# Kernel tuning notes

Hardware: AMD Instinct MI355X
Metric: run time of the kernel (lower is better)

Reference implementation:

```python
import jax, jax.numpy as jnp
import numpy as np

B, S = 2, 1024
ENC_IN, MARK_IN = 21, 4
PRED_LEN, C_OUT = 96, 21
E = 512                 # embedding_dim
INNER = 2 * E           # proj_factor=2.0 (library default; Model does not pass it)
NH = 8                  # mLSTM heads
DH = INNER // NH        # 128
K = 4                   # causal conv1d kernel
BS = 4                  # qkv_proj_blocksize
NHP = INNER // BS       # 256 block-diagonal proj heads
NB = 4                  # num_blocks
EPS = 1e-5


def setup_inputs() -> dict:
    key = jax.random.key(0)
    ks = jax.random.split(key, 24)
    it = iter(range(24))
    def n(shape, s=0.02):
        return jax.random.normal(ks[next(it)], shape, jnp.float32) * s
    return {
        "x_enc": n((B, S, ENC_IN), 1.0),
        "x_mark_enc": n((B, S, MARK_IN), 1.0),
        "x_dec": n((B, PRED_LEN, ENC_IN), 1.0),
        "x_mark_dec": n((B, PRED_LEN, MARK_IN), 1.0),
        "emb_W": n((ENC_IN + MARK_IN, E), 0.05),
        "emb_b": jnp.zeros((E,), jnp.float32),
        "ln_w": jnp.ones((NB, E), jnp.float32),
        "up_W": n((NB, E, 2 * INNER)),
        "conv_W": n((NB, INNER, K), 0.1),
        "conv_b": jnp.zeros((NB, INNER), jnp.float32),
        "q_W": n((NB, NHP, BS, BS), 0.1),
        "k_W": n((NB, NHP, BS, BS), 0.1),
        "v_W": n((NB, NHP, BS, BS), 0.1),
        "ig_W": n((NB, 3 * INNER, NH)),
        "ig_b": jnp.zeros((NB, NH), jnp.float32),
        "fg_W": n((NB, 3 * INNER, NH)),
        "fg_b": jnp.tile(jnp.linspace(3.0, 6.0, NH, dtype=jnp.float32), (NB, 1)),
        "skip": jnp.ones((NB, INNER), jnp.float32),
        "onorm_w": jnp.ones((NB, INNER), jnp.float32),
        "down_W": n((NB, INNER, E)),
        "post_ln_w": jnp.ones((E,), jnp.float32),
        "head_W": n((E, C_OUT), 0.05),
        "head_b": jnp.zeros((C_OUT,), jnp.float32),
    }


def _ln(x, w):
    mu = jnp.mean(x, -1, keepdims=True)
    var = jnp.var(x, -1, keepdims=True)
    return (x - mu) * jax.lax.rsqrt(var + EPS) * w


def _headwise(x, w):
    # block-diagonal LinearHeadwiseExpand: (B,S,INNER) with (NHP,BS,BS) blocks
    xh = x.reshape(x.shape[0], x.shape[1], NHP, BS)
    return jnp.einsum('bshd,hod->bsho', xh, w).reshape(x.shape)


def _block(x, lw, uW, cW, cb, qW, kW, vW, igW, igb, fgW, fgb, sk, ow, dW):
    xn = _ln(x, lw)
    up = xn @ uW                                  # (B,S,2*INNER)
    xm, z = up[..., :INNER], up[..., INNER:]
    # causal depthwise conv1d + SiLU
    xc = jax.lax.conv_general_dilated(
        xm.transpose(0, 2, 1), cW[:, None, :], (1,), [(K - 1, 0)],
        feature_group_count=INNER,
        dimension_numbers=('NCH', 'OIH', 'NCH')).transpose(0, 2, 1) + cb
    xc = jax.nn.silu(xc)
    q = _headwise(xc, qW)
    k = _headwise(xc, kW)
    v = _headwise(xm, vW)
    qkv = jnp.concatenate([q, k, v], -1)          # (B,S,3*INNER)
    ig = (qkv @ igW + igb).transpose(0, 2, 1)     # (B,NH,S)
    fg = (qkv @ fgW + fgb).transpose(0, 2, 1)
    qh = q.reshape(B, S, NH, DH).transpose(0, 2, 1, 3)
    kh = k.reshape(B, S, NH, DH).transpose(0, 2, 1, 3)
    vh = v.reshape(B, S, NH, DH).transpose(0, 2, 1, 3)
    # parallel stabilized mLSTM (exp-gated linear attention)
    log_f = jax.nn.log_sigmoid(fg)
    cs = jnp.cumsum(log_f, -1)                    # (B,NH,S)
    Mmat = cs[..., :, None] - cs[..., None, :]    # (B,NH,S,S) cumulative decay
    tri = jnp.tril(jnp.ones((S, S), bool))
    logD = jnp.where(tri, Mmat + ig[..., None, :], -jnp.inf)
    m = jnp.max(logD, -1, keepdims=True)          # row-wise stabilizer
    D = jnp.exp(logD - m)
    qk = jnp.einsum('bnsd,bntd->bnst', qh, kh) / (DH ** 0.5)
    C = qk * D
    norm = jnp.maximum(jnp.abs(jnp.sum(C, -1, keepdims=True)), jnp.exp(-m))
    h = jnp.einsum('bnst,bntd->bnsd', C / (norm + 1e-6), vh)
    # multi-head layernorm (groupnorm over DH per head), weight, no bias
    hn = (h - jnp.mean(h, -1, keepdims=True)) * jax.lax.rsqrt(jnp.var(h, -1, keepdims=True) + EPS)
    hn = hn.transpose(0, 2, 1, 3).reshape(B, S, INNER) * ow
    hs = (hn + sk * xc) * jax.nn.silu(z)          # learnable skip + output gate
    return x + hs @ dW                            # residual


def reference(x_enc, x_mark_enc, x_dec, x_mark_dec, emb_W, emb_b, ln_w, up_W,
              conv_W, conv_b, q_W, k_W, v_W, ig_W, ig_b, fg_W, fg_b, skip,
              onorm_w, down_W, post_ln_w, head_W, head_b):
    x = jnp.concatenate([x_enc, x_mark_enc], -1) @ emb_W + emb_b
    for i in range(NB):
        x = _block(x, ln_w[i], up_W[i], conv_W[i], conv_b[i], q_W[i], k_W[i],
                   v_W[i], ig_W[i], ig_b[i], fg_W[i], fg_b[i], skip[i],
                   onorm_w[i], down_W[i])
    x = _ln(x, post_ln_w)
    return x[:, -PRED_LEN:, :] @ head_W + head_b
```

## Files before the change

kernel.cpp:

```cpp
#include <hip/hip_runtime.h>
#include <hip/hip_bf16.h>

#define S_LEN 1024
#define E_DIM 512
#define INNER_D 1024
#define NHEAD 8
#define DHEAD 128

typedef unsigned short u16;
typedef unsigned int u32;
typedef __attribute__((ext_vector_type(8))) short short8;
typedef __attribute__((ext_vector_type(4))) float f32x4;

union S8 { short8 v; u16 u[8]; uint4 q; };

__device__ __forceinline__ u16 f2bf(float f) {
  u32 u = __float_as_uint(f);
  u32 r = u + 0x7FFFu + ((u >> 16) & 1u);
  return (u16)(r >> 16);
}
__device__ __forceinline__ float bf2f(u16 u) { return __uint_as_float(((u32)u) << 16); }

__device__ __forceinline__ void gload16(const u16* g, u16* l) {
  __builtin_amdgcn_global_load_lds((const __attribute__((address_space(1))) void*)g,
                                   (__attribute__((address_space(3))) void*)l, 16, 0, 0);
}

__device__ __forceinline__ void prep_transpose(
    const float* __restrict__ in, u16* __restrict__ out, int K, int N,
    int k0, int n0, int t, u16 (*T)[72])
{
  int kr = t >> 2, nseg = (t & 3) * 16;
  const float* src = in + (size_t)(k0 + kr) * N + n0 + nseg;
#pragma unroll
  for (int j = 0; j < 16; j++) T[kr][nseg + j] = f2bf(src[j]);
  __syncthreads();
  int nr = t >> 2, kseg = (t & 3) * 16;
  u32 u[8];
#pragma unroll
  for (int rr = 0; rr < 8; rr++) {
    u32 lo = T[kseg + 2 * rr][nr];
    u32 hi = T[kseg + 2 * rr + 1][nr];
    u[rr] = lo | (hi << 16);
  }
  u16* dst = out + (size_t)(n0 + nr) * K + k0 + kseg;
  uint4 w0 = {u[0], u[1], u[2], u[3]};
  uint4 w1 = {u[4], u[5], u[6], u[7]};
  *(uint4*)dst = w0;
  *(uint4*)(dst + 8) = w1;
}

__global__ __launch_bounds__(256) void prep_kernel(
    const float* __restrict__ up_W, u16* __restrict__ upWt,
    const float* __restrict__ down_W, u16* __restrict__ dnWt,
    const float* __restrict__ igW, const float* __restrict__ fgW,
    u16* __restrict__ ghi, u16* __restrict__ glo,
    const float* __restrict__ xe, const float* __restrict__ xmk,
    const float* __restrict__ eW, const float* __restrict__ eb,
    float* __restrict__ x)
{
  __shared__ u16 T[64][72];
  __shared__ float in_s[25];
  int id = blockIdx.x;
  int t = threadIdx.x;
  if (id < 1024) {
    int bx = id & 7, rest = id >> 3;
    int by = rest & 31, L = rest >> 5;
    prep_transpose(up_W + (size_t)L * 512 * 2048, upWt + (size_t)L * 1048576,
                   512, 2048, bx * 64, by * 64, t, T);
  } else if (id < 1536) {
    int id2 = id - 1024;
    int bx = id2 & 15, rest = id2 >> 4;
    int by = rest & 7, L = rest >> 3;
    prep_transpose(down_W + (size_t)L * 1024 * 512, dnWt + (size_t)L * 524288,
                   1024, 512, bx * 64, by * 64, t, T);
  } else if (id < 2304) {
    int id3 = id - 1536;
    int bx = id3 % 12, rest = id3 / 12;
    int n = rest & 15, L = rest >> 4;
    int k = bx * 256 + t;
    const float* W = ((n < 8) ? igW : fgW) + (size_t)L * 24576;
    float v = W[(size_t)k * 8 + (n & 7)];
    u16 h = f2bf(v);
    u16 l = f2bf(v - bf2f(h));
    size_t o = ((size_t)L * 16 + n) * 3072 + k;
    ghi[o] = h;
    glo[o] = l;
  } else {
    int row = id - 2304;
    if (t < 21) in_s[t] = xe[row * 21 + t];
    else if (t < 25) in_s[t] = xmk[row * 4 + t - 21];
    __syncthreads();
#pragma unroll
    for (int rep = 0; rep < 2; rep++) {
      int e = t + rep * 256;
      float acc = eb[e];
#pragma unroll
      for (int i = 0; i < 25; i++) acc += in_s[i] * eW[i * E_DIM + e];
      x[(size_t)row * E_DIM + e] = acc;
    }
  }
}

__global__ __launch_bounds__(256) void ln_kernel(
    const float* __restrict__ x, const float* __restrict__ w, u16* __restrict__ out)
{
  int row = blockIdx.x, tid = threadIdx.x;
  const float* xr = x + (size_t)row * E_DIM;
  float2 v = *(const float2*)(xr + tid * 2);
  float s = v.x + v.y, q = v.x * v.x + v.y * v.y;
#pragma unroll
  for (int off = 32; off; off >>= 1) { s += __shfl_xor(s, off); q += __shfl_xor(q, off); }
  __shared__ float ssum[4], ssq[4];
  int wv = tid >> 6;
  if ((tid & 63) == 0) { ssum[wv] = s; ssq[wv] = q; }
  __syncthreads();
  s = ssum[0] + ssum[1] + ssum[2] + ssum[3];
  q = ssq[0] + ssq[1] + ssq[2] + ssq[3];
  float mu = s * (1.f / E_DIM);
  float var = q * (1.f / E_DIM) - mu * mu;
  float rs = rsqrtf(var + 1e-5f);
  int e = tid * 2;
  ushort2 o;
  o.x = f2bf((v.x - mu) * rs * w[e]);
  o.y = f2bf((v.y - mu) * rs * w[e + 1]);
  *(ushort2*)(out + (size_t)row * E_DIM + e) = o;
}

__global__ __launch_bounds__(256) void lnhead_kernel(
    const float* __restrict__ x, const float* __restrict__ w,
    const float* __restrict__ hW, const float* __restrict__ hb,
    float* __restrict__ out)
{
  int ridx = blockIdx.x;
  int b = ridx / 96, r = ridx % 96;
  int row = b * S_LEN + (S_LEN - 96) + r;
  int tid = threadIdx.x;
  const float* xr = x + (size_t)row * E_DIM;
  float2 v = *(const float2*)(xr + tid * 2);
  float s = v.x + v.y, q = v.x * v.x + v.y * v.y;
#pragma unroll
  for (int off = 32; off; off >>= 1) { s += __shfl_xor(s, off); q += __shfl_xor(q, off); }
  __shared__ float ssum[4], ssq[4];
  __shared__ float lnv[512];
  __shared__ float part[8][32];
  int wv = tid >> 6;
  if ((tid & 63) == 0) { ssum[wv] = s; ssq[wv] = q; }
  __syncthreads();
  s = ssum[0] + ssum[1] + ssum[2] + ssum[3];
  q = ssq[0] + ssq[1] + ssq[2] + ssq[3];
  float mu = s * (1.f / E_DIM);
  float var = q * (1.f / E_DIM) - mu * mu;
  float rs = rsqrtf(var + 1e-5f);
  int e = tid * 2;
  lnv[e]     = (v.x - mu) * rs * w[e];
  lnv[e + 1] = (v.y - mu) * rs * w[e + 1];
  __syncthreads();
  int n = tid & 31, sl = tid >> 5;
  float p = 0.f;
  if (n < 21) {
#pragma unroll 8
    for (int kk = 0; kk < 64; kk++)
      p += lnv[sl * 64 + kk] * hW[(sl * 64 + kk) * 21 + n];
  }
  part[sl][n] = p;
  __syncthreads();
  if (tid < 21) {
    float acc = hb[tid];
#pragma unroll
    for (int j = 0; j < 8; j++) acc += part[j][tid];
    out[ridx * 21 + tid] = acc;
  }
}

__global__ __launch_bounds__(256) void gemm_bf16_split64(
    const u16* __restrict__ A, const u16* __restrict__ Bt,
    float* __restrict__ C0, u16* __restrict__ C1,
    int M, int N, int K, int split_col, int ldc)
{
  __shared__ u16 As0[128 * 64], As1[128 * 64], As2[128 * 64];
  __shared__ u16 Bs0[128 * 64], Bs1[128 * 64], Bs2[128 * 64];
  const int tid = threadIdx.x;
  const int row0 = blockIdx.y * 128, col0 = blockIdx.x * 128;
  const int wave = tid >> 6, lane = tid & 63;
  const int wr = wave >> 1, wc = wave & 1;
  const int lm = lane & 15, lq = lane >> 4;
  const int lr8 = lane >> 3;
  const int cg8 = (lane & 7) ^ lr8;
  f32x4 acc[4][4] = {};
  const u16* Abase = A + (size_t)(row0 + lr8) * K + cg8 * 8;
  const u16* Bbase = Bt + (size_t)(col0 + lr8) * K + cg8 * 8;
  const int key = lm & 7;

#define STG_UP(AS, BS, K0) do { \
  _Pragma("unroll") for (int i = 0; i < 4; i++) \
    gload16(Abase + (size_t)((wave * 4 + i) * 8) * K + (K0), &AS[(wave * 4 + i) * 512]); \
  _Pragma("unroll") for (int i = 0; i < 4; i++) \
    gload16(Bbase + (size_t)((wave * 4 + i) * 8) * K + (K0), &BS[(wave * 4 + i) * 512]); \
} while (0)

#define CMP_UP(AS, BS) do { \
  _Pragma("unroll") for (int kc = 0; kc < 2; kc++) { \
    short8 af[4], bfv[4]; \
    _Pragma("unroll") for (int i = 0; i < 4; i++) \
      af[i] = *(const short8*)&AS[(wr * 64 + i * 16 + lm) * 64 + (((kc * 4 + lq) ^ key) * 8)]; \
    _Pragma("unroll") for (int j = 0; j < 4; j++) \
      bfv[j] = *(const short8*)&BS[(wc * 64 + j * 16 + lm) * 64 + (((kc * 4 + lq) ^ key) * 8)]; \
    _Pragma("unroll") for (int i = 0; i < 4; i++) \
      _Pragma("unroll") for (int j = 0; j < 4; j++) \
        acc[i][j] = __builtin_amdgcn_mfma_f32_16x16x32_bf16(af[i], bfv[j], acc[i][j], 0, 0, 0); \
  } \
} while (0)

  STG_UP(As0, Bs0, 0);
  asm volatile("" ::: "memory");
  STG_UP(As1, Bs1, 64);
  asm volatile("" ::: "memory");
  STG_UP(As2, Bs2, 128);
#pragma unroll
  for (int t = 0; t < 8; t++) {
    if (t <= 5)       asm volatile("s_waitcnt vmcnt(16)" ::: "memory");
    else if (t == 6)  asm volatile("s_waitcnt vmcnt(8)" ::: "memory");
    else              asm volatile("s_waitcnt vmcnt(0)" ::: "memory");
    __builtin_amdgcn_sched_barrier(0);
    __builtin_amdgcn_s_barrier();
    if ((t % 3) == 0)      CMP_UP(As0, Bs0);
    else if ((t % 3) == 1) CMP_UP(As1, Bs1);
    else                   CMP_UP(As2, Bs2);
    __builtin_amdgcn_s_barrier();
    if (t + 3 < 8) {
      if ((t % 3) == 0)      STG_UP(As0, Bs0, (t + 3) * 64);
      else if ((t % 3) == 1) STG_UP(As1, Bs1, (t + 3) * 64);
      else                   STG_UP(As2, Bs2, (t + 3) * 64);
    }
  }
#undef STG_UP
#undef CMP_UP

  const bool toC1 = (col0 >= split_col);
#pragma unroll
  for (int i = 0; i < 4; i++) {
#pragma unroll
    for (int j = 0; j < 4; j++) {
      int col = col0 - (toC1 ? split_col : 0) + wc * 64 + j * 16 + lm;
#pragma unroll
      for (int r = 0; r < 4; r++) {
        int row = row0 + wr * 64 + i * 16 + lq * 4 + r;
        if (toC1) C1[(size_t)row * ldc + col] = f2bf(acc[i][j][r]);
        else C0[(size_t)row * ldc + col] = acc[i][j][r];
      }
    }
  }
}

__global__ __launch_bounds__(256) void gemm_bf16_32(
    const u16* __restrict__ A, const u16* __restrict__ Bt,
    float* __restrict__ C, int M, int N, int K, int ldc)
{
  __shared__ u16 As0[64 * 128], As1[64 * 128], As2[64 * 128];
  __shared__ u16 Bs0[64 * 128], Bs1[64 * 128], Bs2[64 * 128];
  const int tid = threadIdx.x;
  const int row0 = blockIdx.y * 64, col0 = blockIdx.x * 64;
  const int wave = tid >> 6, lane = tid & 63;
  const int wr = wave >> 1, wc = wave & 1;
  const int lm = lane & 15, lq = lane >> 4;
  const int lr16 = lane >> 4;
  const int ls16 = lane & 15;
  f32x4 acc[2][2] = {};

#define STAGE_DN(AS, BS, K0) do { \
  _Pragma("unroll") for (int i = 0; i < 4; i++) { \
    int rA = (wave * 4 + i) * 4 + lr16; \
    int cgk = ls16 ^ (rA & 15); \
    gload16(A + (size_t)(row0 + rA) * K + (K0) + cgk * 8, &AS[(wave * 4 + i) * 512]); \
  } \
  _Pragma("unroll") for (int i = 0; i < 4; i++) { \
    int rB = (wave * 4 + i) * 4 + lr16; \
    int cgk = ls16 ^ (rB & 15); \
    gload16(Bt + (size_t)(col0 + rB) * K + (K0) + cgk * 8, &BS[(wave * 4 + i) * 512]); \
  } \
} while (0)

#define COMPUTE_DN(AS, BS) do { \
  _Pragma("unroll") for (int kc = 0; kc < 4; kc++) { \
    short8 af[2], bfv[2]; \
    _Pragma("unroll") for (int i = 0; i < 2; i++) \
      af[i] = *(const short8*)&AS[(wr * 32 + i * 16 + lm) * 128 + (((kc * 4 + lq) ^ lm) * 8)]; \
    _Pragma("unroll") for (int j = 0; j < 2; j++) \
      bfv[j] = *(const short8*)&BS[(wc * 32 + j * 16 + lm) * 128 + (((kc * 4 + lq) ^ lm) * 8)]; \
    _Pragma("unroll") for (int i = 0; i < 2; i++) \
      _Pragma("unroll") for (int j = 0; j < 2; j++) \
        acc[i][j] = __builtin_amdgcn_mfma_f32_16x16x32_bf16(af[i], bfv[j], acc[i][j], 0, 0, 0); \
  } \
} while (0)

  STAGE_DN(As0, Bs0, 0);
  asm volatile("" ::: "memory");
  STAGE_DN(As1, Bs1, 128);
  asm volatile("" ::: "memory");
  STAGE_DN(As2, Bs2, 256);
#pragma unroll
  for (int t = 0; t < 8; t++) {
    if (t <= 5)       asm volatile("s_waitcnt vmcnt(16)" ::: "memory");
    else if (t == 6)  asm volatile("s_waitcnt vmcnt(8)" ::: "memory");
    else              asm volatile("s_waitcnt vmcnt(0)" ::: "memory");
    __builtin_amdgcn_sched_barrier(0);
    __builtin_amdgcn_s_barrier();
    if ((t % 3) == 0)      COMPUTE_DN(As0, Bs0);
    else if ((t % 3) == 1) COMPUTE_DN(As1, Bs1);
    else                   COMPUTE_DN(As2, Bs2);
    __builtin_amdgcn_s_barrier();
    if (t + 3 < 8) {
      if ((t % 3) == 0)      STAGE_DN(As0, Bs0, (t + 3) * 128);
      else if ((t % 3) == 1) STAGE_DN(As1, Bs1, (t + 3) * 128);
      else                   STAGE_DN(As2, Bs2, (t + 3) * 128);
    }
  }
#undef STAGE_DN
#undef COMPUTE_DN

#pragma unroll
  for (int i = 0; i < 2; i++) {
#pragma unroll
    for (int j = 0; j < 2; j++) {
      int col = col0 + wc * 32 + j * 16 + lm;
#pragma unroll
      for (int r = 0; r < 4; r++) {
        int row = row0 + wr * 32 + i * 16 + lq * 4 + r;
        C[(size_t)row * ldc + col] += acc[i][j][r];
      }
    }
  }
}

__global__ __launch_bounds__(256) void convqkv_kernel(
    const float* __restrict__ xm,
    const float* __restrict__ cw, const float* __restrict__ cb,
    const float* __restrict__ qw, const float* __restrict__ kw, const float* __restrict__ vw,
    float* __restrict__ xc, u16* __restrict__ q, u16* __restrict__ k, u16* __restrict__ v,
    u16* __restrict__ vt)
{
  int r0 = blockIdx.x * 8;
  int s0 = r0 & (S_LEN - 1);
  int g = threadIdx.x;
  int c0 = g * 4;
  const float* base = xm + (size_t)r0 * INNER_D + c0;

  float4 xv[11];
#pragma unroll
  for (int j = 0; j < 11; j++) {
    int ts = s0 - 3 + j;
    float4 t = {0.f, 0.f, 0.f, 0.f};
    if (ts >= 0) t = *(const float4*)(base + (ptrdiff_t)(j - 3) * INNER_D);
    xv[j] = t;
  }
  float cwv[4][4];
#pragma unroll
  for (int c = 0; c < 4; c++)
#pragma unroll
    for (int kk = 0; kk < 4; kk++) cwv[c][kk] = cw[(c0 + c) * 4 + kk];
  float cbv[4] = {cb[c0], cb[c0 + 1], cb[c0 + 2], cb[c0 + 3]};
  const float* qg = qw + g * 16;
  const float* kg = kw + g * 16;
  const float* vg = vw + g * 16;
  float qwv[16], kwv[16], vwv[16];
#pragma unroll
  for (int i = 0; i < 16; i++) { qwv[i] = qg[i]; kwv[i] = kg[i]; vwv[i] = vg[i]; }

  u32 vt_pack[4][4];

#pragma unroll
  for (int i = 0; i < 8; i++) {
    float a0 = cbv[0], a1 = cbv[1], a2 = cbv[2], a3 = cbv[3];
#pragma unroll
    for (int kk = 0; kk < 4; kk++) {
      float4 xvv = xv[i + kk];
      a0 += xvv.x * cwv[0][kk];
      a1 += xvv.y * cwv[1][kk];
      a2 += xvv.z * cwv[2][kk];
      a3 += xvv.w * cwv[3][kk];
    }
    a0 = a0 / (1.f + __expf(-a0));
    a1 = a1 / (1.f + __expf(-a1));
    a2 = a2 / (1.f + __expf(-a2));
    a3 = a3 / (1.f + __expf(-a3));
    float4 accv = {a0, a1, a2, a3};
    *(float4*)(xc + (size_t)(r0 + i) * INNER_D + c0) = accv;

    float xcv[4] = {a0, a1, a2, a3};
    float xmv[4] = {xv[i + 3].x, xv[i + 3].y, xv[i + 3].z, xv[i + 3].w};
    ushort4 qs, ks, vs;
    u16* qp = (u16*)&qs; u16* kp = (u16*)&ks; u16* vp = (u16*)&vs;
#pragma unroll
    for (int o = 0; o < 4; o++) {
      float aq = 0.f, ak = 0.f, av = 0.f;
#pragma unroll
      for (int d = 0; d < 4; d++) {
        aq += xcv[d] * qwv[o * 4 + d];
        ak += xcv[d] * kwv[o * 4 + d];
        av += xmv[d] * vwv[o * 4 + d];
      }
      qp[o] = f2bf(aq); kp[o] = f2bf(ak);
      u16 vv = f2bf(av);
      vp[o] = vv;
      if ((i & 1) == 0) vt_pack[o][i >> 1] = (u32)vv;
      else              vt_pack[o][i >> 1] |= ((u32)vv) << 16;
    }
    size_t off = (size_t)(r0 + i) * INNER_D + c0;
    *(ushort4*)(q + off) = qs;
    *(ushort4*)(k + off) = ks;
    *(ushort4*)(v + off) = vs;
  }
  u16* vtb = vt + ((size_t)((r0 >> 10) * INNER_D + c0)) * S_LEN + s0;
#pragma unroll
  for (int c = 0; c < 4; c++) {
    uint4 wv4 = {vt_pack[c][0], vt_pack[c][1], vt_pack[c][2], vt_pack[c][3]};
    *(uint4*)(vtb + (size_t)c * S_LEN) = wv4;
  }
}

__global__ __launch_bounds__(256) void gates_mfma_kernel(
    const u16* __restrict__ q, const u16* __restrict__ k, const u16* __restrict__ v,
    const u16* __restrict__ whi, const u16* __restrict__ wlo,
    const float* __restrict__ igb, const float* __restrict__ fgb,
    float* __restrict__ ig, float* __restrict__ fg)
{
  const int blk2 = blockIdx.x;
  const int blk = blk2 >> 1, half = blk2 & 1;
  const int tid = threadIdx.x;
  const int wave = tid >> 6, lane = tid & 63;
  const int lm = lane & 15, lq = lane >> 4;
  const int grow = blk * 16 + lm;
  const u16* parts[3] = {q, k, v};
  f32x4 acc = {};
#pragma unroll 4
  for (int kc = 0; kc < 12; kc++) {
    int k0 = half * 1536 + wave * 384 + kc * 32;
    int part = k0 >> 10;
    int idx = (k0 & 1023) + lq * 8;
    S8 a, bh_, bl_;
    a.q = *(const uint4*)(parts[part] + (size_t)grow * INNER_D + idx);
    bh_.q = *(const uint4*)(whi + (size_t)lm * 3072 + k0 + lq * 8);
    bl_.q = *(const uint4*)(wlo + (size_t)lm * 3072 + k0 + lq * 8);
    __builtin_amdgcn_s_setprio(1);
    acc = __builtin_amdgcn_mfma_f32_16x16x32_bf16(a.v, bh_.v, acc, 0, 0, 0);
    acc = __builtin_amdgcn_mfma_f32_16x16x32_bf16(a.v, bl_.v, acc, 0, 0, 0);
    __builtin_amdgcn_s_setprio(0);
  }
  __shared__ float red[4][16][17];
#pragma unroll
  for (int r = 0; r < 4; r++) red[wave][lq * 4 + r][lm] = acc[r];
  __syncthreads();
  if (wave == 0) {
#pragma unroll
    for (int r = 0; r < 4; r++) {
      int row = lq * 4 + r;
      float sum = red[0][row][lm] + red[1][row][lm] + red[2][row][lm] + red[3][row][lm];
      int growr = blk * 16 + row;
      int b = growr >> 10, s = growr & (S_LEN - 1);
      if (lm < 8) {
        float bias = (half == 0) ? igb[lm] : 0.f;
        ig[half * 16384 + ((size_t)(b * NHEAD + lm) << 10) + s] = sum + bias;
      } else {
        float bias = (half == 0) ? fgb[lm - 8] : 0.f;
        fg[half * 16384 + ((size_t)(b * NHEAD + (lm - 8)) << 10) + s] = sum + bias;
      }
    }
  }
}

__global__ __launch_bounds__(1024) void scan_kernel(
    const float* __restrict__ ig, const float* __restrict__ fg,
    float* __restrict__ a, float* __restrict__ rm, float* __restrict__ enm)
{
  int bh = blockIdx.x;
  int t = threadIdx.x;
  int lane = t & 63, wv = t >> 6;
  __shared__ float sw[16];
  size_t o = ((size_t)bh << 10) + t;
  float f = fg[o] + fg[16384 + o];
  float lf = (f >= 0.f) ? -log1pf(__expf(-f)) : f - log1pf(__expf(f));
  float v = lf;
#pragma unroll
  for (int off = 1; off < 64; off <<= 1) {
    float u = __shfl_up(v, off);
    if (lane >= off) v += u;
  }
  if (lane == 63) sw[wv] = v;
  __syncthreads();
  float pre = 0.f;
  for (int w = 0; w < wv; w++) pre += sw[w];
  float cs = v + pre;
  float av = (ig[o] + ig[16384 + o]) - cs;
  a[o] = __expf(av);
  float m = av;
#pragma unroll
  for (int off = 1; off < 64; off <<= 1) {
    float u = __shfl_up(m, off);
    if (lane >= off) m = fmaxf(m, u);
  }
  __syncthreads();
  if (lane == 63) sw[wv] = m;
  __syncthreads();
  float pm = -3.4e38f;
  for (int w = 0; w < wv; w++) pm = fmaxf(pm, sw[w]);
  float rmx = fmaxf(m, pm);
  rm[o] = rmx;
  enm[o] = __expf(-(cs + rmx));
}

__device__ __constant__ int c_qp[15] = {7, 7, 7, 6, 6, 6, 5, 5, 4, 4, 3, 3, 2, 1, 0};
__device__ __constant__ int c_k0[15] = {0, 6,11, 0, 5,10, 0, 6, 0, 5, 0, 4, 0, 0, 0};
__device__ __constant__ int c_k1[15] = {6,11,16, 5,10,14, 6,12, 5,10, 4, 8, 6, 4, 2};
__device__ __constant__ int c_md[15] = {1, 2, 3, 1, 2, 3, 1, 2, 1, 2, 1, 2, 0, 0, 0};

#define HP_SLOT 1310720
#define SC_SLOT 10240

__global__ __launch_bounds__(512) void attn_mfma_kernel(
    const u16* __restrict__ qhg, const u16* __restrict__ khg, const u16* __restrict__ vtg,
    const float* __restrict__ a_arr, const float* __restrict__ rm_arr, const float* __restrict__ enm_arr,
    const float* __restrict__ xc, const u16* __restrict__ zh,
    const float* __restrict__ skip, const float* __restrict__ onw,
    u16* __restrict__ hs, float* __restrict__ hpart, float* __restrict__ scpart)
{
  const int bh = blockIdx.x;
  const int job = blockIdx.y;
  const int qp = c_qp[job], k0t = c_k0[job], k1t = c_k1[job], mode = c_md[job];
  const int b = bh >> 3, h = bh & 7;
  const int s0 = qp * 128;
  const int tid = threadIdx.x;
  const int wave = tid >> 6, lane = tid & 63;
  const int lm = lane & 15, lq = lane >> 4;
  const size_t rowbase = (size_t)b * S_LEN;
  const int c0 = h * DHEAD;

  __shared__ u16 Ks0[64 * 128], Ks1[64 * 128];
  __shared__ u16 Vt0[128 * 64], Vt1[128 * 64];
  __shared__ u16 Ws[128 * 72];

  short8 aq[4];
  {
    const u16* qpp = qhg + (rowbase + s0 + wave * 16 + lm) * INNER_D + c0 + lq * 8;
#pragma unroll
    for (int kc = 0; kc < 4; kc++) {
      S8 tmp; tmp.q = *(const uint4*)(qpp + kc * 32);
      aq[kc] = tmp.v;
    }
  }
  const float scale = 0.08838834764831845f;
  float rmv[4], er[4];
#pragma unroll
  for (int r = 0; r < 4; r++) {
    rmv[r] = rm_arr[(size_t)bh * S_LEN + s0 + wave * 16 + lq * 4 + r];
    er[r] = scale * __expf(-rmv[r]);
  }

  S8 onesu;
#pragma unroll
  for (int j = 0; j < 8; j++) onesu.u[j] = 0x3F80;
  const short8 ones8 = onesu.v;

  f32x4 accH[8] = {};
  f32x4 accS = {};
  const int lr16 = lane >> 4;
  const int ls16 = lane & 15;
  const int lr8 = lane >> 3;
  const int cgv = (lane & 7) ^ lr8;
  const u16* vtbase = vtg + ((size_t)b * INNER_D + c0) * S_LEN;

  float ae0[4], ae1[4];

#define PREF(KS, VS, AE, T0) do { \
  _Pragma("unroll") for (int j = 0; j < 2; j++) { \
    int rK = (wave * 2 + j) * 4 + lr16; \
    int cgk = ls16 ^ (rK & 7); \
    gload16(khg + (rowbase + (T0) + rK) * INNER_D + c0 + cgk * 8, &KS[(wave * 2 + j) * 512]); \
  } \
  _Pragma("unroll") for (int j = 0; j < 2; j++) { \
    int rV = (wave * 2 + j) * 8 + lr8; \
    gload16(vtbase + (size_t)rV * S_LEN + (T0) + cgv * 8, &VS[(wave * 2 + j) * 512]); \
  } \
  _Pragma("unroll") for (int cb = 0; cb < 4; cb++) \
    AE[cb] = a_arr[(size_t)bh * S_LEN + (T0) + cb * 16 + lm]; \
} while (0)

#define QK_STEP(KS, PACC) do { \
  __builtin_amdgcn_s_setprio(1); \
  _Pragma("unroll") for (int kc = 0; kc < 4; kc++) \
    _Pragma("unroll") for (int cb = 0; cb < 4; cb++) { \
      short8 bk = *(const short8*)&KS[(cb * 16 + lm) * 128 + (((kc * 4 + lq) ^ (lm & 7)) * 8)]; \
      PACC[cb] = __builtin_amdgcn_mfma_f32_16x16x32_bf16(aq[kc], bk, PACC[cb], 0, 0, 0); \
    } \
  __builtin_amdgcn_s_setprio(0); \
} while (0)

#define W_PV(AE, VT, T0, PACC, MSK) do { \
  _Pragma("unroll") for (int cb = 0; cb < 4; cb++) { \
    float ec = AE[cb]; \
    _Pragma("unroll") for (int r = 0; r < 4; r++) { \
      float wv = PACC[cb][r] * ec * er[r]; \
      if (MSK) { \
        int colg = (T0) + cb * 16 + lm; \
        int rowg = s0 + wave * 16 + lq * 4 + r; \
        if (colg > rowg) wv = 0.f; \
      } \
      Ws[(wave * 16 + lq * 4 + r) * 72 + cb * 16 + lm] = f2bf(wv); \
    } \
  } \
  __builtin_amdgcn_s_setprio(1); \
  _Pragma("unroll") for (int kc = 0; kc < 2; kc++) { \
    short8 aw = *(const short8*)&Ws[(wave * 16 + lm) * 72 + kc * 32 + lq * 8]; \
    accS = __builtin_amdgcn_mfma_f32_16x16x32_bf16(aw, ones8, accS, 0, 0, 0); \
    _Pragma("unroll") for (int nb = 0; nb < 8; nb++) { \
      short8 bv = *(const short8*)&VT[(nb * 16 + lm) * 64 + (((kc * 4 + lq) ^ (lm & 7)) * 8)]; \
      accH[nb] = __builtin_amdgcn_mfma_f32_16x16x32_bf16(aw, bv, accH[nb], 0, 0, 0); \
    } \
  } \
  __builtin_amdgcn_s_setprio(0); \
} while (0)

  int kt = k0t;
  PREF(Ks0, Vt0, ae0, kt * 64);
  asm volatile("" ::: "memory");
  if (kt + 1 < k1t) PREF(Ks1, Vt1, ae1, (kt + 1) * 64);

  while (true) {
    {
      if (kt + 1 < k1t) asm volatile("s_waitcnt vmcnt(8)" ::: "memory");
      else              asm volatile("s_waitcnt vmcnt(0)" ::: "memory");
      __builtin_amdgcn_sched_barrier(0);
      __builtin_amdgcn_s_barrier();
      f32x4 pacc[4] = {};
      QK_STEP(Ks0, pacc);
      bool msk = (kt * 64 >= s0);
      W_PV(ae0, Vt0, kt * 64, pacc, msk);
      __builtin_amdgcn_s_barrier();
      if (kt + 2 < k1t) PREF(Ks0, Vt0, ae0, (kt + 2) * 64);
      kt++;
      if (kt >= k1t) break;
    }
    {
      if (kt + 1 < k1t) asm volatile("s_waitcnt vmcnt(8)" ::: "memory");
      else              asm volatile("s_waitcnt vmcnt(0)" ::: "memory");
      __builtin_amdgcn_sched_barrier(0);
      __builtin_amdgcn_s_barrier();
      f32x4 pacc[4] = {};
      QK_STEP(Ks1, pacc);
      bool msk = (kt * 64 >= s0);
      W_PV(ae1, Vt1, kt * 64, pacc, msk);
      __builtin_amdgcn_s_barrier();
      if (kt + 2 < k1t) PREF(Ks1, Vt1, ae1, (kt + 2) * 64);
      kt++;
      if (kt >= k1t) break;
    }
  }
#undef PREF
#undef QK_STEP
#undef W_PV

  if (mode != 0) {
    int slot = mode - 1;
    int qr = qp - 3;
    float* Hp = hpart + (size_t)slot * HP_SLOT + ((size_t)(bh * 5 + qr)) * 16384;
    float* sp = scpart + slot * SC_SLOT + (bh * 5 + qr) * 128;
#pragma unroll
    for (int r = 0; r < 4; r++) {
      int row = wave * 16 + lq * 4 + r;
      if (lm == 0) sp[row] = accS[r];
#pragma unroll
      for (int nb = 0; nb < 8; nb++)
        Hp[row * 128 + nb * 16 + lm] = accH[nb][r];
    }
    return;
  }

  float inv[4], muv[4], rsv[4];
#pragma unroll
  for (int r = 0; r < 4; r++) {
    int rowg = s0 + wave * 16 + lq * 4 + r;
    float nrm = fmaxf(fabsf(accS[r]), enm_arr[(size_t)bh * S_LEN + rowg]);
    inv[r] = 1.f / (nrm + 1e-6f);
  }
#pragma unroll
  for (int r = 0; r < 4; r++) {
    float s = 0.f, qq = 0.f;
#pragma unroll
    for (int nb = 0; nb < 8; nb++) {
      float hv = accH[nb][r] * inv[r];
      accH[nb][r] = hv;
      s += hv; qq += hv * hv;
    }
    s += __shfl_xor(s, 1); s += __shfl_xor(s, 2); s += __shfl_xor(s, 4); s += __shfl_xor(s, 8);
    qq += __shfl_xor(qq, 1); qq += __shfl_xor(qq, 2); qq += __shfl_xor(qq, 4); qq += __shfl_xor(qq, 8);
    float mu = s * (1.f / DHEAD);
    float var = qq * (1.f / DHEAD) - mu * mu;
    muv[r] = mu;
    rsv[r] = rsqrtf(var + 1e-5f);
  }
  float ow[8], sk[8];
#pragma unroll
  for (int nb = 0; nb < 8; nb++) {
    ow[nb] = onw[c0 + nb * 16 + lm];
    sk[nb] = skip[c0 + nb * 16 + lm];
  }
#pragma unroll
  for (int r = 0; r < 4; r++) {
    int rowg = s0 + wave * 16 + lq * 4 + r;
    size_t base = (rowbase + rowg) * INNER_D + c0;
#pragma unroll
    for (int nb = 0; nb < 8; nb++) {
      int d = nb * 16 + lm;
      float xcv = xc[base + d];
      float zv = bf2f(zh[base + d]);
      float hn = (accH[nb][r] - muv[r]) * rsv[r] * ow[nb] + sk[nb] * xcv;
      float o = hn * (zv / (1.f + __expf(-zv)));
      hs[base + d] = f2bf(o);
    }
  }
}

__global__ __launch_bounds__(256) void attn_combine_kernel(
    const float* __restrict__ hpart, const float* __restrict__ scpart,
    const float* __restrict__ enm,
    const float* __restrict__ xc, const u16* __restrict__ zh,
    const float* __restrict__ skip, const float* __restrict__ onw,
    u16* __restrict__ hs)
{
  int wave = threadIdx.x >> 6, lane = threadIdx.x & 63;
  int gid = blockIdx.x * 4 + wave;
  int bh = gid / 640;
  int rr = gid % 640;
  int qr = rr >> 7, row = rr & 127;
  int b = bh >> 3, hh = bh & 7;
  int s = (qr + 3) * 128 + row;
  int nsl = (qr >= 3) ? 3 : 2;
  size_t off = (((size_t)(bh * 5 + qr)) * 128 + row) * 128 + lane * 2;
  int sidx = (bh * 5 + qr) * 128 + row;
  float hx = 0.f, hy = 0.f, sc = 0.f;
  for (int sl = 0; sl < nsl; sl++) {
    float2 hp = *(const float2*)(hpart + (size_t)sl * HP_SLOT + off);
    hx += hp.x; hy += hp.y;
    sc += scpart[sl * SC_SLOT + sidx];
  }
  float nrm = fmaxf(fabsf(sc), enm[(size_t)bh * S_LEN + s]);
  float inv = 1.f / (nrm + 1e-6f);
  hx *= inv; hy *= inv;
  float sm = hx + hy, sq = hx * hx + hy * hy;
#pragma unroll
  for (int off2 = 32; off2; off2 >>= 1) { sm += __shfl_xor(sm, off2); sq += __shfl_xor(sq, off2); }
  float mu = sm * (1.f / DHEAD);
  float var = sq * (1.f / DHEAD) - mu * mu;
  float rs = rsqrtf(var + 1e-5f);
  int c0 = hh * DHEAD + lane * 2;
  size_t base = ((size_t)(b * S_LEN + s)) * INNER_D + c0;
  float2 xc2 = *(const float2*)(xc + base);
  ushort2 z2u = *(const ushort2*)(zh + base);
  float z2x = bf2f(z2u.x), z2y = bf2f(z2u.y);
  float skx = skip[c0], sky = skip[c0 + 1];
  float owx = onw[c0],  owy = onw[c0 + 1];
  ushort2 o;
  o.x = f2bf(((hx - mu) * rs * owx + skx * xc2.x) * (z2x / (1.f + __expf(-z2x))));
  o.y = f2bf(((hy - mu) * rs * owy + sky * xc2.y) * (z2y / (1.f + __expf(-z2y))));
  *(ushort2*)(hs + base) = o;
}

extern "C" void kernel_launch(void* const* d_in, const int* in_sizes, int n_in,
                              void* d_out, int out_size, void* d_ws, size_t ws_size,
                              hipStream_t stream)
{
  const float* x_enc   = (const float*)d_in[0];
  const float* x_mark  = (const float*)d_in[1];
  const float* emb_W   = (const float*)d_in[4];
  const float* emb_b   = (const float*)d_in[5];
  const float* ln_w    = (const float*)d_in[6];
  const float* up_W    = (const float*)d_in[7];
  const float* conv_W  = (const float*)d_in[8];
  const float* conv_b  = (const float*)d_in[9];
  const float* q_W     = (const float*)d_in[10];
  const float* k_W     = (const float*)d_in[11];
  const float* v_W     = (const float*)d_in[12];
  const float* ig_W    = (const float*)d_in[13];
  const float* ig_b    = (const float*)d_in[14];
  const float* fg_W    = (const float*)d_in[15];
  const float* fg_b    = (const float*)d_in[16];
  const float* skip_w  = (const float*)d_in[17];
  const float* onorm_w = (const float*)d_in[18];
  const float* down_W  = (const float*)d_in[19];
  const float* post_ln = (const float*)d_in[20];
  const float* head_W  = (const float*)d_in[21];
  const float* head_b  = (const float*)d_in[22];

  float* p = (float*)d_ws;
  float* x    = p; p += 1048576;
  float* xm   = p; p += 2097152;
  float* xc   = p; p += 2097152;
  float* igb_ = p; p += 32768;
  float* fgb_ = p; p += 32768;
  float* ab   = p; p += 16384;
  float* rmb  = p; p += 16384;
  float* enmb = p; p += 16384;
  u16* qhb = (u16*)p; p += 1048576;
  u16* khb = (u16*)p; p += 1048576;
  u16* vhb = (u16*)p; p += 1048576;
  u16* zh  = (u16*)p; p += 1048576;
  u16* xnh = (u16*)p; p += 524288;
  u16* upWtA = (u16*)p; p += 2097152;
  u16* dnWtA = (u16*)p; p += 1048576;
  u16* gtwH = (u16*)p; p += 98304;
  u16* gtwL = (u16*)p; p += 98304;
  float* hpart = p; p += 3932160;
  float* scpart = p; p += 32768;
  u16* vtg = (u16*)p; p += 1048576;
  u16* hsbh = (u16*)xm;

  prep_kernel<<<4352, 256, 0, stream>>>(
      up_W, upWtA, down_W, dnWtA, ig_W, fg_W, gtwH, gtwL,
      x_enc, x_mark, emb_W, emb_b, x);

  for (int L = 0; L < 4; L++) {
    ln_kernel<<<2048, 256, 0, stream>>>(x, ln_w + L * 512, xnh);
    gemm_bf16_split64<<<dim3(16, 16), 256, 0, stream>>>(
        xnh, upWtA + (size_t)L * 1048576, xm, zh, 2048, 2048, 512, 1024, 1024);
    convqkv_kernel<<<256, 256, 0, stream>>>(
        xm, conv_W + L * 4096, conv_b + L * 1024,
        q_W + L * 4096, k_W + L * 4096, v_W + L * 4096,
        xc, qhb, khb, vhb, vtg);
    gates_mfma_kernel<<<256, 256, 0, stream>>>(
        qhb, khb, vhb, gtwH + (size_t)L * 49152, gtwL + (size_t)L * 49152,
        ig_b + L * 8, fg_b + L * 8, igb_, fgb_);
    scan_kernel<<<16, 1024, 0, stream>>>(igb_, fgb_, ab, rmb, enmb);
    attn_mfma_kernel<<<dim3(16, 15), 512, 0, stream>>>(
        qhb, khb, vtg, ab, rmb, enmb, xc, zh,
        skip_w + L * 1024, onorm_w + L * 1024, hsbh, hpart, scpart);
    attn_combine_kernel<<<2560, 256, 0, stream>>>(
        hpart, scpart, enmb, xc, zh, skip_w + L * 1024, onorm_w + L * 1024, hsbh);
    gemm_bf16_32<<<dim3(8, 32), 256, 0, stream>>>(
        hsbh, dnWtA + (size_t)L * 524288, x, 2048, 512, 1024, 512);
  }

  lnhead_kernel<<<192, 256, 0, stream>>>(x, post_ln, head_W, head_b, (float*)d_out);
}
```

Measured before the change: 415.5 us.

## Fuse gate scan into attention kernel and vectorize layernorm rows per wave

Removes the separate scan_kernel launch: every attention block recomputes the forget-gate cumulative sum, decay exponentials and running max for its head in shared memory, and stores the stabilizer only for its own query tile. Decay factors are read from LDS instead of being prefetched from global memory, so the vmcnt wait counts are lowered. The layernorm kernel now handles one row per wave with float4 loads and 16-byte stores, using a quarter of the blocks. The trade-off is redundant scan work across the 15 job blocks per head and more LDS use, in exchange for one fewer launch and fewer global round trips per layer.

```diff
diff --git a/kernel.cpp b/kernel.cpp
--- a/kernel.cpp
+++ b/kernel.cpp
@@ -105,26 +105,30 @@
 __global__ __launch_bounds__(256) void ln_kernel(
     const float* __restrict__ x, const float* __restrict__ w, u16* __restrict__ out)
 {
-  int row = blockIdx.x, tid = threadIdx.x;
-  const float* xr = x + (size_t)row * E_DIM;
-  float2 v = *(const float2*)(xr + tid * 2);
-  float s = v.x + v.y, q = v.x * v.x + v.y * v.y;
-#pragma unroll
-  for (int off = 32; off; off >>= 1) { s += __shfl_xor(s, off); q += __shfl_xor(q, off); }
-  __shared__ float ssum[4], ssq[4];
-  int wv = tid >> 6;
-  if ((tid & 63) == 0) { ssum[wv] = s; ssq[wv] = q; }
-  __syncthreads();
-  s = ssum[0] + ssum[1] + ssum[2] + ssum[3];
-  q = ssq[0] + ssq[1] + ssq[2] + ssq[3];
+  int row = blockIdx.x * 4 + (threadIdx.x >> 6);
+  int lane = threadIdx.x & 63;
+  const float* xr = x + (size_t)row * E_DIM + lane * 8;
+  float4 a = *(const float4*)xr;
+  float4 b = *(const float4*)(xr + 4);
+  float s = a.x + a.y + a.z + a.w + b.x + b.y + b.z + b.w;
+  float q = a.x * a.x + a.y * a.y + a.z * a.z + a.w * a.w
+          + b.x * b.x + b.y * b.y + b.z * b.z + b.w * b.w;
+#pragma unroll
+  for (int off = 1; off < 64; off <<= 1) { s += __shfl_xor(s, off); q += __shfl_xor(q, off); }
   float mu = s * (1.f / E_DIM);
   float var = q * (1.f / E_DIM) - mu * mu;
   float rs = rsqrtf(var + 1e-5f);
-  int e = tid * 2;
-  ushort2 o;
-  o.x = f2bf((v.x - mu) * rs * w[e]);
-  o.y = f2bf((v.y - mu) * rs * w[e + 1]);
-  *(ushort2*)(out + (size_t)row * E_DIM + e) = o;
+  const float* wr = w + lane * 8;
+  S8 o;
+  o.u[0] = f2bf((a.x - mu) * rs * wr[0]);
+  o.u[1] = f2bf((a.y - mu) * rs * wr[1]);
+  o.u[2] = f2bf((a.z - mu) * rs * wr[2]);
+  o.u[3] = f2bf((a.w - mu) * rs * wr[3]);
+  o.u[4] = f2bf((b.x - mu) * rs * wr[4]);
+  o.u[5] = f2bf((b.y - mu) * rs * wr[5]);
+  o.u[6] = f2bf((b.z - mu) * rs * wr[6]);
+  o.u[7] = f2bf((b.w - mu) * rs * wr[7]);
+  *(uint4*)(out + (size_t)row * E_DIM + lane * 8) = o.q;
 }
 
 __global__ __launch_bounds__(256) void lnhead_kernel(
@@ -469,46 +473,6 @@
   }
 }
 
-__global__ __launch_bounds__(1024) void scan_kernel(
-    const float* __restrict__ ig, const float* __restrict__ fg,
-    float* __restrict__ a, float* __restrict__ rm, float* __restrict__ enm)
-{
-  int bh = blockIdx.x;
-  int t = threadIdx.x;
-  int lane = t & 63, wv = t >> 6;
-  __shared__ float sw[16];
-  size_t o = ((size_t)bh << 10) + t;
-  float f = fg[o] + fg[16384 + o];
-  float lf = (f >= 0.f) ? -log1pf(__expf(-f)) : f - log1pf(__expf(f));
-  float v = lf;
-#pragma unroll
-  for (int off = 1; off < 64; off <<= 1) {
-    float u = __shfl_up(v, off);
-    if (lane >= off) v += u;
-  }
-  if (lane == 63) sw[wv] = v;
-  __syncthreads();
-  float pre = 0.f;
-  for (int w = 0; w < wv; w++) pre += sw[w];
-  float cs = v + pre;
-  float av = (ig[o] + ig[16384 + o]) - cs;
-  a[o] = __expf(av);
-  float m = av;
-#pragma unroll
-  for (int off = 1; off < 64; off <<= 1) {
-    float u = __shfl_up(m, off);
-    if (lane >= off) m = fmaxf(m, u);
-  }
-  __syncthreads();
-  if (lane == 63) sw[wv] = m;
-  __syncthreads();
-  float pm = -3.4e38f;
-  for (int w = 0; w < wv; w++) pm = fmaxf(pm, sw[w]);
-  float rmx = fmaxf(m, pm);
-  rm[o] = rmx;
-  enm[o] = __expf(-(cs + rmx));
-}
-
 __device__ __constant__ int c_qp[15] = {7, 7, 7, 6, 6, 6, 5, 5, 4, 4, 3, 3, 2, 1, 0};
 __device__ __constant__ int c_k0[15] = {0, 6,11, 0, 5,10, 0, 6, 0, 5, 0, 4, 0, 0, 0};
 __device__ __constant__ int c_k1[15] = {6,11,16, 5,10,14, 6,12, 5,10, 4, 8, 6, 4, 2};
@@ -519,10 +483,11 @@
 
 __global__ __launch_bounds__(512) void attn_mfma_kernel(
     const u16* __restrict__ qhg, const u16* __restrict__ khg, const u16* __restrict__ vtg,
-    const float* __restrict__ a_arr, const float* __restrict__ rm_arr, const float* __restrict__ enm_arr,
+    const float* __restrict__ ig_arr, const float* __restrict__ fg_arr,
     const float* __restrict__ xc, const u16* __restrict__ zh,
     const float* __restrict__ skip, const float* __restrict__ onw,
-    u16* __restrict__ hs, float* __restrict__ hpart, float* __restrict__ scpart)
+    u16* __restrict__ hs, float* __restrict__ hpart, float* __restrict__ scpart,
+    float* __restrict__ enmp)
 {
   const int bh = blockIdx.x;
   const int job = blockIdx.y;
@@ -538,6 +503,9 @@
   __shared__ u16 Ks0[64 * 128], Ks1[64 * 128];
   __shared__ u16 Vt0[128 * 64], Vt1[128 * 64];
   __shared__ u16 Ws[128 * 72];
+  __shared__ float sa[1024];
+  __shared__ float sws[16], swm[16];
+  __shared__ float srm[128], senm[128];
 
   short8 aq[4];
   {
@@ -548,11 +516,65 @@
       aq[kc] = tmp.v;
     }
   }
+
+  {
+    float vsc[2], igv[2], css[2], msc[2];
+#pragma unroll
+    for (int c = 0; c < 2; c++) {
+      int vt = c * 512 + tid;
+      size_t o = ((size_t)bh << 10) + vt;
+      float f = fg_arr[o] + fg_arr[16384 + o];
+      igv[c] = ig_arr[o] + ig_arr[16384 + o];
+      float lf = (f >= 0.f) ? -log1pf(__expf(-f)) : f - log1pf(__expf(f));
+      float v = lf;
+#pragma unroll
+      for (int off = 1; off < 64; off <<= 1) {
+        float u = __shfl_up(v, off);
+        if (lane >= off) v += u;
+      }
+      if (lane == 63) sws[c * 8 + (tid >> 6)] = v;
+      vsc[c] = v;
+    }
+    __syncthreads();
+#pragma unroll
+    for (int c = 0; c < 2; c++) {
+      int vt = c * 512 + tid;
+      int wvv = c * 8 + (tid >> 6);
+      float pre = 0.f;
+      for (int u = 0; u < wvv; u++) pre += sws[u];
+      float cs = vsc[c] + pre;
+      float av = igv[c] - cs;
+      sa[vt] = __expf(av);
+      float m = av;
+#pragma unroll
+      for (int off = 1; off < 64; off <<= 1) {
+        float u = __shfl_up(m, off);
+        if (lane >= off) m = fmaxf(m, u);
+      }
+      if (lane == 63) swm[wvv] = m;
+      css[c] = cs; msc[c] = m;
+    }
+    __syncthreads();
+#pragma unroll
+    for (int c = 0; c < 2; c++) {
+      int vt = c * 512 + tid;
+      int wvv = c * 8 + (tid >> 6);
+      float pm = -3.4e38f;
+      for (int u = 0; u < wvv; u++) pm = fmaxf(pm, swm[u]);
+      float rmx = fmaxf(msc[c], pm);
+      if (vt >= s0 && vt < s0 + 128) {
+        srm[vt - s0] = rmx;
+        senm[vt - s0] = __expf(-(css[c] + rmx));
+      }
+    }
+    __syncthreads();
+  }
+
   const float scale = 0.08838834764831845f;
   float rmv[4], er[4];
 #pragma unroll
   for (int r = 0; r < 4; r++) {
-    rmv[r] = rm_arr[(size_t)bh * S_LEN + s0 + wave * 16 + lq * 4 + r];
+    rmv[r] = srm[wave * 16 + lq * 4 + r];
     er[r] = scale * __expf(-rmv[r]);
   }
 
@@ -569,9 +591,7 @@
   const int cgv = (lane & 7) ^ lr8;
   const u16* vtbase = vtg + ((size_t)b * INNER_D + c0) * S_LEN;
 
-  float ae0[4], ae1[4];
-
-#define PREF(KS, VS, AE, T0) do { \
+#define PREF(KS, VS, T0) do { \
   _Pragma("unroll") for (int j = 0; j < 2; j++) { \
     int rK = (wave * 2 + j) * 4 + lr16; \
     int cgk = ls16 ^ (rK & 7); \
@@ -581,8 +601,6 @@
     int rV = (wave * 2 + j) * 8 + lr8; \
     gload16(vtbase + (size_t)rV * S_LEN + (T0) + cgv * 8, &VS[(wave * 2 + j) * 512]); \
   } \
-  _Pragma("unroll") for (int cb = 0; cb < 4; cb++) \
-    AE[cb] = a_arr[(size_t)bh * S_LEN + (T0) + cb * 16 + lm]; \
 } while (0)
 
 #define QK_STEP(KS, PACC) do { \
@@ -595,9 +613,9 @@
   __builtin_amdgcn_s_setprio(0); \
 } while (0)
 
-#define W_PV(AE, VT, T0, PACC, MSK) do { \
+#define W_PV(VT, T0, PACC, MSK) do { \
   _Pragma("unroll") for (int cb = 0; cb < 4; cb++) { \
-    float ec = AE[cb]; \
+    float ec = sa[(T0) + cb * 16 + lm]; \
     _Pragma("unroll") for (int r = 0; r < 4; r++) { \
       float wv = PACC[cb][r] * ec * er[r]; \
       if (MSK) { \
@@ -621,36 +639,36 @@
 } while (0)
 
   int kt = k0t;
-  PREF(Ks0, Vt0, ae0, kt * 64);
+  PREF(Ks0, Vt0, kt * 64);
   asm volatile("" ::: "memory");
-  if (kt + 1 < k1t) PREF(Ks1, Vt1, ae1, (kt + 1) * 64);
+  if (kt + 1 < k1t) PREF(Ks1, Vt1, (kt + 1) * 64);
 
   while (true) {
     {
-      if (kt + 1 < k1t) asm volatile("s_waitcnt vmcnt(8)" ::: "memory");
+      if (kt + 1 < k1t) asm volatile("s_waitcnt vmcnt(4)" ::: "memory");
       else              asm volatile("s_waitcnt vmcnt(0)" ::: "memory");
       __builtin_amdgcn_sched_barrier(0);
       __builtin_amdgcn_s_barrier();
       f32x4 pacc[4] = {};
       QK_STEP(Ks0, pacc);
       bool msk = (kt * 64 >= s0);
-      W_PV(ae0, Vt0, kt * 64, pacc, msk);
+      W_PV(Vt0, kt * 64, pacc, msk);
       __builtin_amdgcn_s_barrier();
-      if (kt + 2 < k1t) PREF(Ks0, Vt0, ae0, (kt + 2) * 64);
+      if (kt + 2 < k1t) PREF(Ks0, Vt0, (kt + 2) * 64);
       kt++;
       if (kt >= k1t) break;
     }
     {
-      if (kt + 1 < k1t) asm volatile("s_waitcnt vmcnt(8)" ::: "memory");
+      if (kt + 1 < k1t) asm volatile("s_waitcnt vmcnt(4)" ::: "memory");
       else              asm volatile("s_waitcnt vmcnt(0)" ::: "memory");
       __builtin_amdgcn_sched_barrier(0);
       __builtin_amdgcn_s_barrier();
       f32x4 pacc[4] = {};
       QK_STEP(Ks1, pacc);
       bool msk = (kt * 64 >= s0);
-      W_PV(ae1, Vt1, kt * 64, pacc, msk);
+      W_PV(Vt1, kt * 64, pacc, msk);
       __builtin_amdgcn_s_barrier();
-      if (kt + 2 < k1t) PREF(Ks1, Vt1, ae1, (kt + 2) * 64);
+      if (kt + 2 < k1t) PREF(Ks1, Vt1, (kt + 2) * 64);
       kt++;
       if (kt >= k1t) break;
     }
@@ -664,10 +682,14 @@
     int qr = qp - 3;
     float* Hp = hpart + (size_t)slot * HP_SLOT + ((size_t)(bh * 5 + qr)) * 16384;
     float* sp = scpart + slot * SC_SLOT + (bh * 5 + qr) * 128;
+    float* ep = enmp + (bh * 5 + qr) * 128;
 #pragma unroll
     for (int r = 0; r < 4; r++) {
       int row = wave * 16 + lq * 4 + r;
-      if (lm == 0) sp[row] = accS[r];
+      if (lm == 0) {
+        sp[row] = accS[r];
+        if (slot == 0) ep[row] = senm[row];
+      }
 #pragma unroll
       for (int nb = 0; nb < 8; nb++)
         Hp[row * 128 + nb * 16 + lm] = accH[nb][r];
@@ -678,8 +700,8 @@
   float inv[4], muv[4], rsv[4];
 #pragma unroll
   for (int r = 0; r < 4; r++) {
-    int rowg = s0 + wave * 16 + lq * 4 + r;
-    float nrm = fmaxf(fabsf(accS[r]), enm_arr[(size_t)bh * S_LEN + rowg]);
+    int row = wave * 16 + lq * 4 + r;
+    float nrm = fmaxf(fabsf(accS[r]), senm[row]);
     inv[r] = 1.f / (nrm + 1e-6f);
   }
 #pragma unroll
@@ -722,7 +744,7 @@
 
 __global__ __launch_bounds__(256) void attn_combine_kernel(
     const float* __restrict__ hpart, const float* __restrict__ scpart,
-    const float* __restrict__ enm,
+    const float* __restrict__ enmp,
     const float* __restrict__ xc, const u16* __restrict__ zh,
     const float* __restrict__ skip, const float* __restrict__ onw,
     u16* __restrict__ hs)
@@ -743,7 +765,7 @@
     hx += hp.x; hy += hp.y;
     sc += scpart[sl * SC_SLOT + sidx];
   }
-  float nrm = fmaxf(fabsf(sc), enm[(size_t)bh * S_LEN + s]);
+  float nrm = fmaxf(fabsf(sc), enmp[sidx]);
   float inv = 1.f / (nrm + 1e-6f);
   hx *= inv; hy *= inv;
   float sm = hx + hy, sq = hx * hx + hy * hy;
@@ -797,9 +819,7 @@
   float* xc   = p; p += 2097152;
   float* igb_ = p; p += 32768;
   float* fgb_ = p; p += 32768;
-  float* ab   = p; p += 16384;
-  float* rmb  = p; p += 16384;
-  float* enmb = p; p += 16384;
+  float* enmp = p; p += 16384;
   u16* qhb = (u16*)p; p += 1048576;
   u16* khb = (u16*)p; p += 1048576;
   u16* vhb = (u16*)p; p += 1048576;
@@ -819,7 +839,7 @@
       x_enc, x_mark, emb_W, emb_b, x);
 
   for (int L = 0; L < 4; L++) {
-    ln_kernel<<<2048, 256, 0, stream>>>(x, ln_w + L * 512, xnh);
+    ln_kernel<<<512, 256, 0, stream>>>(x, ln_w + L * 512, xnh);
     gemm_bf16_split64<<<dim3(16, 16), 256, 0, stream>>>(
         xnh, upWtA + (size_t)L * 1048576, xm, zh, 2048, 2048, 512, 1024, 1024);
     convqkv_kernel<<<256, 256, 0, stream>>>(
@@ -829,12 +849,11 @@
     gates_mfma_kernel<<<256, 256, 0, stream>>>(
         qhb, khb, vhb, gtwH + (size_t)L * 49152, gtwL + (size_t)L * 49152,
         ig_b + L * 8, fg_b + L * 8, igb_, fgb_);
-    scan_kernel<<<16, 1024, 0, stream>>>(igb_, fgb_, ab, rmb, enmb);
     attn_mfma_kernel<<<dim3(16, 15), 512, 0, stream>>>(
-        qhb, khb, vtg, ab, rmb, enmb, xc, zh,
-        skip_w + L * 1024, onorm_w + L * 1024, hsbh, hpart, scpart);
+        qhb, khb, vtg, igb_, fgb_, xc, zh,
+        skip_w + L * 1024, onorm_w + L * 1024, hsbh, hpart, scpart, enmp);
     attn_combine_kernel<<<2560, 256, 0, stream>>>(
-        hpart, scpart, enmb, xc, zh, skip_w + L * 1024, onorm_w + L * 1024, hsbh);
+        hpart, scpart, enmp, xc, zh, skip_w + L * 1024, onorm_w + L * 1024, hsbh);
     gemm_bf16_32<<<dim3(8, 32), 256, 0, stream>>>(
         hsbh, dnWtA + (size_t)L * 524288, x, 2048, 512, 1024, 512);
   }
```

New measurement: 415.0 us. Within noise of the previous version (-0.1%).
